# Kernel optimization log

Hardware: AMD Instinct MI355X
Metric: run time of the kernel (lower is better)

The kernel has to match this reference:

```python
import jax, jax.numpy as jnp
import numpy as np

B, L = 4, 2048
D_MODEL, D_STATE, D_CONV, N_BLOCKS = 128, 16, 8, 6
EXPAND = 2
D_INNER = EXPAND * D_MODEL          # 256
DT_RANK = (D_MODEL + 15) // 16      # 8
CONV_K = 7                          # pre_conv kernel


def setup_inputs() -> dict:
    key = jax.random.key(0)
    ks = jax.random.split(key, 10)
    f = lambda k, s: jax.random.normal(k, s, jnp.float32)
    sc = 0.02
    A_init = jnp.broadcast_to(
        jnp.log(jnp.arange(1, D_STATE + 1, dtype=jnp.float32)),
        (N_BLOCKS, D_INNER, D_STATE)) + 0.0
    return {
        "x": f(ks[0], (B, L, 1)),
        "pre_conv_w": f(ks[1], (D_MODEL, 1, CONV_K)) * sc,
        "pre_conv_b": jnp.zeros((D_MODEL,), jnp.float32),
        "ln_w": jnp.ones((N_BLOCKS, D_MODEL), jnp.float32),
        "ln_b": jnp.zeros((N_BLOCKS, D_MODEL), jnp.float32),
        "W_in": f(ks[2], (N_BLOCKS, 2 * D_INNER, D_MODEL)) * sc,
        "conv_w": f(ks[3], (N_BLOCKS, D_INNER, 1, D_CONV)) * sc,  # depthwise OIH
        "conv_b": jnp.zeros((N_BLOCKS, D_INNER), jnp.float32),
        "W_x": f(ks[4], (N_BLOCKS, DT_RANK + 2 * D_STATE, D_INNER)) * sc,
        "W_dt": f(ks[5], (N_BLOCKS, D_INNER, DT_RANK)) * sc,
        "b_dt": jnp.full((N_BLOCKS, D_INNER), -4.6, jnp.float32),  # softplus ~ 0.01
        "A_log": A_init,
        "D_skip": jnp.ones((N_BLOCKS, D_INNER), jnp.float32),
        "W_out": f(ks[6], (N_BLOCKS, D_MODEL, D_INNER)) * sc,
        "out_w": f(ks[7], (1, D_MODEL)) * sc,
        "out_b": jnp.zeros((1,), jnp.float32),
    }


def _layernorm(x, w, b, eps=1e-5):
    m = jnp.mean(x, axis=-1, keepdims=True)
    v = jnp.mean(jnp.square(x - m), axis=-1, keepdims=True)
    return (x - m) * jax.lax.rsqrt(v + eps) * w + b


def _mamba(x, W_in, cw, cb, W_x, W_dt, b_dt, A_log, D_skip, W_out):
    # x: (B, L, D_MODEL)
    xz = jnp.einsum('bld,ed->ble', x, W_in)            # (B,L,2E)
    xi, z = jnp.split(xz, 2, axis=-1)
    # depthwise causal conv over time
    xc = jax.lax.conv_general_dilated(
        xi.transpose(0, 2, 1), cw, window_strides=(1,),
        padding=[(D_CONV - 1, 0)],
        dimension_numbers=('NCH', 'OIH', 'NCH'),
        feature_group_count=D_INNER) + cb[None, :, None]
    xc = jax.nn.silu(xc).transpose(0, 2, 1)            # (B,L,E)
    dbl = jnp.einsum('ble,re->blr', xc, W_x)
    dt = dbl[..., :DT_RANK]
    Bm = dbl[..., DT_RANK:DT_RANK + D_STATE]           # (B,L,N)
    Cm = dbl[..., DT_RANK + D_STATE:]                  # (B,L,N)
    delta = jax.nn.softplus(jnp.einsum('blr,er->ble', dt, W_dt) + b_dt)
    A = -jnp.exp(A_log)                                # (E,N)

    def step(h, inp):
        d, b, c, u = inp                               # (B,E),(B,N),(B,N),(B,E)
        h = h * jnp.exp(d[..., None] * A) + (d * u)[..., None] * b[:, None, :]
        return h, jnp.einsum('ben,bn->be', h, c)

    h0 = jnp.zeros((x.shape[0], D_INNER, D_STATE), x.dtype)
    xs = (delta.transpose(1, 0, 2), Bm.transpose(1, 0, 2),
          Cm.transpose(1, 0, 2), xc.transpose(1, 0, 2))
    _, ys = jax.lax.scan(step, h0, xs)                 # ys: (L,B,E)
    y = ys.transpose(1, 0, 2) + D_skip * xc
    y = y * jax.nn.silu(z)
    return jnp.einsum('ble,de->bld', y, W_out)


def reference(x, pre_conv_w, pre_conv_b, ln_w, ln_b, W_in, conv_w, conv_b,
              W_x, W_dt, b_dt, A_log, D_skip, W_out, out_w, out_b):
    # pre_conv (1 -> d_model), SAME padding, then exact GELU
    h = jax.lax.conv_general_dilated(
        x.transpose(0, 2, 1), pre_conv_w, window_strides=(1,),
        padding=[(CONV_K // 2, CONV_K // 2)],
        dimension_numbers=('NCH', 'OIH', 'NCH')) + pre_conv_b[None, :, None]
    h = jax.nn.gelu(h, approximate=False).transpose(0, 2, 1)  # (B,L,D)

    def block(carry, p):
        lw, lb, Wi, cw, cb, Wx, Wdt, bdt, Alog, Dsk, Wo = p
        y = _mamba(_layernorm(carry, lw, lb), Wi, cw, cb, Wx, Wdt, bdt, Alog, Dsk, Wo)
        return carry + y, None                         # dropout is identity (eval)

    h, _ = jax.lax.scan(block, h, (ln_w, ln_b, W_in, conv_w, conv_b,
                                   W_x, W_dt, b_dt, A_log, D_skip, W_out))
    return (jnp.einsum('bld,od->blo', h, out_w) + out_b)[..., 0]  # (B,L)
```

## Files before the change

### kernel.cpp

```cpp
#include <hip/hip_runtime.h>
#include <hip/hip_bf16.h>
#include <hip/hip_cooperative_groups.h>
#include <math.h>

namespace cg = cooperative_groups;

#define BB 4
#define LL 2048
#define DM 128
#define DI 256
#define DS 16
#define DTR 8
#define NB 6
#define KPRE 7
#define KC 8
#define NC 128
#define CT 16
#define NCHUNK (BB*NC)
#define BL (BB*LL)
#define SU 4

typedef __attribute__((ext_vector_type(8))) short short8v;
typedef __attribute__((ext_vector_type(4))) short short4v;
typedef __attribute__((ext_vector_type(4))) float f32x4;

__device__ __forceinline__ void store_bf16x4(__hip_bfloat16* p, float a, float b, float c, float d) {
    __hip_bfloat16 t[4] = {__float2bfloat16(a), __float2bfloat16(b),
                           __float2bfloat16(c), __float2bfloat16(d)};
    *(short4v*)p = *(const short4v*)t;
}
__device__ __forceinline__ float4 load_bf16x4(const __hip_bfloat16* p) {
    short4v raw = *(const short4v*)p;
    const __hip_bfloat16* t = (const __hip_bfloat16*)&raw;
    return make_float4(__bfloat162float(t[0]), __bfloat162float(t[1]),
                       __bfloat162float(t[2]), __bfloat162float(t[3]));
}
__device__ __forceinline__ void load_bf16x16(const __hip_bfloat16* p, float* o) {
    short8v a = *(const short8v*)p;
    short8v b = *(const short8v*)(p + 8);
    const __hip_bfloat16* ta = (const __hip_bfloat16*)&a;
    const __hip_bfloat16* tb = (const __hip_bfloat16*)&b;
#pragma unroll
    for (int i = 0; i < 8; ++i) { o[i] = __bfloat162float(ta[i]); o[8 + i] = __bfloat162float(tb[i]); }
}
__device__ __forceinline__ void store_bf16x16(__hip_bfloat16* p, const float* v) {
    __hip_bfloat16 t[16];
#pragma unroll
    for (int i = 0; i < 16; ++i) t[i] = __float2bfloat16(v[i]);
    *(short8v*)p = *(const short8v*)t;
    *(short8v*)(p + 8) = *(const short8v*)(t + 8);
}


__device__ __forceinline__ void dev_preconv(int idx,
    const float* __restrict__ x, const float* __restrict__ w, const float* __restrict__ bias,
    float* __restrict__ h, const float* __restrict__ Wi, const float* __restrict__ Wo,
    __hip_bfloat16* __restrict__ wi, __hip_bfloat16* __restrict__ wo) {
    int d = idx & (DM - 1);
    int l = (idx >> 7) & (LL - 1);
    int b = idx >> 18;
    float acc = bias[d];
#pragma unroll
    for (int k = 0; k < KPRE; ++k) {
        int pos = l + k - 3;
        float xv = (pos >= 0 && pos < LL) ? x[b * LL + pos] : 0.f;
        acc = fmaf(xv, w[d * KPRE + k], acc);
    }
    h[idx] = 0.5f * acc * (1.f + erff(acc * 0.70710678118654752f));
    if (idx < NB * 2 * DI * DM) wi[idx] = __float2bfloat16(Wi[idx]);
    if (idx < NB * DM * DI)     wo[idx] = __float2bfloat16(Wo[idx]);
}

__device__ __forceinline__ void dev_phaseA(int chunk, int tid, int epoch,
    const float* __restrict__ h, const float* __restrict__ lw, const float* __restrict__ lb,
    const __hip_bfloat16* __restrict__ Wi,
    const float* __restrict__ cw, const float* __restrict__ cbs,
    const float* __restrict__ Wx, const float* __restrict__ Wdt, const float* __restrict__ bdt,
    const float* __restrict__ A_log,
    __hip_bfloat16* __restrict__ Pst, __hip_bfloat16* __restrict__ hend,
    __hip_bfloat16* __restrict__ hincl, int* __restrict__ flags,
    __hip_bfloat16* As, __hip_bfloat16 (*xi_s)[DI],
    float (*xc_s)[DI], float (*dl_s)[DI], float (*bc_s)[32],
    __hip_bfloat16 (*z_s)[DI], __hip_bfloat16 (*hin_s)[DS]) {
    int c = chunk & (NC - 1);
    int b = chunk >> 7;
    int wave = tid >> 6, lane = tid & 63;
    for (int it = 0; it < 8; ++it) {
        int lr = wave * 8 + it;
        int tl = c * CT + lr - 16;
        int sw = (lr & 7) << 3;
        if (tl >= 0) {
            int t = b * LL + tl;
            float v0 = h[t * DM + lane];
            float v1 = h[t * DM + lane + 64];
            float s = v0 + v1;
#pragma unroll
            for (int off = 32; off; off >>= 1) s += __shfl_xor(s, off);
            float mean = s * (1.f / 128.f);
            float d0 = v0 - mean, d1 = v1 - mean;
            float q = d0 * d0 + d1 * d1;
#pragma unroll
            for (int off = 32; off; off >>= 1) q += __shfl_xor(q, off);
            float rstd = rsqrtf(q * (1.f / 128.f) + 1e-5f);
            As[lr * 128 + (lane ^ sw)]        = __float2bfloat16(d0 * rstd * lw[lane] + lb[lane]);
            As[lr * 128 + ((lane + 64) ^ sw)] = __float2bfloat16(d1 * rstd * lw[lane + 64] + lb[lane + 64]);
        } else {
            As[lr * 128 + (lane ^ sw)]        = __float2bfloat16(0.f);
            As[lr * 128 + ((lane + 64) ^ sw)] = __float2bfloat16(0.f);
        }
    }
    __syncthreads();
    {
        int r = lane & 15, kh = lane >> 4;
        short8v af[2][4];
#pragma unroll
        for (int mf = 0; mf < 2; ++mf)
#pragma unroll
            for (int k = 0; k < 4; ++k) {
                int row = mf * 16 + r;
                int cbk = k * 4 + kh;
                af[mf][k] = *(const short8v*)&As[row * 128 + ((cbk ^ (row & 7)) << 3)];
            }
        int nBase = wave * 128;
        for (int nf = 0; nf < 8; ++nf) {
            short8v bfr[4];
#pragma unroll
            for (int k = 0; k < 4; ++k)
                bfr[k] = *(const short8v*)&Wi[(size_t)(nBase + nf * 16 + r) * DM + k * 32 + kh * 8];
            if (wave < 2) {
                f32x4 acc0 = {}, acc1 = {};
#pragma unroll
                for (int k = 0; k < 4; ++k) {
                    acc0 = __builtin_amdgcn_mfma_f32_16x16x32_bf16(af[0][k], bfr[k], acc0, 0, 0, 0);
                    acc1 = __builtin_amdgcn_mfma_f32_16x16x32_bf16(af[1][k], bfr[k], acc1, 0, 0, 0);
                }
#pragma unroll
                for (int rg = 0; rg < 4; ++rg) {
                    xi_s[kh * 4 + rg][nBase + nf * 16 + r]      = __float2bfloat16(acc0[rg]);
                    xi_s[16 + kh * 4 + rg][nBase + nf * 16 + r] = __float2bfloat16(acc1[rg]);
                }
            } else {
                f32x4 acc1 = {};
#pragma unroll
                for (int k = 0; k < 4; ++k)
                    acc1 = __builtin_amdgcn_mfma_f32_16x16x32_bf16(af[1][k], bfr[k], acc1, 0, 0, 0);
#pragma unroll
                for (int rg = 0; rg < 4; ++rg)
                    z_s[kh * 4 + rg][(nBase - 256) + nf * 16 + r] = __float2bfloat16(acc1[rg]);
            }
        }
    }
    __syncthreads();
    for (int i = 0; i < 4; ++i) {
        int lt = wave * 4 + i;
        float xv[4];
        for (int j = 0; j < 4; ++j) {
            int e = lane + 64 * j;
            float4 c0 = *(const float4*)&cw[e * KC];
            float4 c1 = *(const float4*)&cw[e * KC + 4];
            float wts[8] = {c0.x, c0.y, c0.z, c0.w, c1.x, c1.y, c1.z, c1.w};
            float acc = cbs[e];
#pragma unroll
            for (int k = 0; k < KC; ++k)
                acc = fmaf(__bfloat162float(xi_s[lt + 9 + k][e]), wts[k], acc);
            xv[j] = acc / (1.f + __expf(-acc));
            xc_s[lt][e] = xv[j];
        }
        float dt8[8];
        float bcv = 0.f;
#pragma unroll
        for (int o = 0; o < 40; ++o) {
            const float* w = &Wx[o * DI];
            float s = xv[0] * w[lane];
            s = fmaf(xv[1], w[lane + 64], s);
            s = fmaf(xv[2], w[lane + 128], s);
            s = fmaf(xv[3], w[lane + 192], s);
#pragma unroll
            for (int off = 32; off; off >>= 1) s += __shfl_xor(s, off);
            if (o < 8) dt8[o] = s;
            else if (lane == o - 8) bcv = s;
        }
        if (lane < 32) bc_s[lt][lane] = bcv;
        for (int j = 0; j < 4; ++j) {
            int e = lane + 64 * j;
            float s = bdt[e];
#pragma unroll
            for (int r = 0; r < 8; ++r) s = fmaf(dt8[r], Wdt[e * 8 + r], s);
            dl_s[lt][e] = fmaxf(s, 0.f) + log1pf(__expf(-fabsf(s)));
        }
    }
    __syncthreads();
    int e = tid;
    {
        float d16[CT], u16[CT];
#pragma unroll
        for (int l = 0; l < CT; ++l) { d16[l] = dl_s[l][e]; u16[l] = xc_s[l][e]; }
        for (int ng = 0; ng < 4; ++ng) {
            float4 al = *(const float4*)&A_log[e * DS + 4 * ng];
            float Aen[4] = {-__expf(al.x), -__expf(al.y), -__expf(al.z), -__expf(al.w)};
            float hh[4] = {}, Pl[4] = {1.f, 1.f, 1.f, 1.f};
#pragma unroll
            for (int l = 0; l < CT; ++l) {
                float du = d16[l] * u16[l];
                float4 bm = *(const float4*)&bc_s[l][4 * ng];
                float a0 = __expf(d16[l] * Aen[0]);
                float a1 = __expf(d16[l] * Aen[1]);
                float a2 = __expf(d16[l] * Aen[2]);
                float a3 = __expf(d16[l] * Aen[3]);
                hh[0] = fmaf(hh[0], a0, du * bm.x);
                hh[1] = fmaf(hh[1], a1, du * bm.y);
                hh[2] = fmaf(hh[2], a2, du * bm.z);
                hh[3] = fmaf(hh[3], a3, du * bm.w);
                Pl[0] *= a0; Pl[1] *= a1; Pl[2] *= a2; Pl[3] *= a3;
            }
            size_t oidx = (((size_t)(b * NC + c)) * DI + e) * DS + 4 * ng;
            store_bf16x4(&Pst[oidx], Pl[0], Pl[1], Pl[2], Pl[3]);
            store_bf16x4(&hend[oidx], hh[0], hh[1], hh[2], hh[3]);
        }
    }
    __threadfence();
    __syncthreads();
    if (tid == 0)
        __hip_atomic_store(&flags[b * NC + c], 2 * epoch,
                           __ATOMIC_RELEASE, __HIP_MEMORY_SCOPE_AGENT);
    float hacc[16], Pacc[16];
#pragma unroll
    for (int n = 0; n < 16; ++n) { hacc[n] = 0.f; Pacc[n] = 1.f; }
    int j = c - 1;
    while (j >= 0) {
        int j2 = (j >= 1) ? j - 1 : j;
        int f1, f0;
        do {
            f1 = __hip_atomic_load(&flags[b * NC + j],  __ATOMIC_ACQUIRE, __HIP_MEMORY_SCOPE_AGENT);
            f0 = __hip_atomic_load(&flags[b * NC + j2], __ATOMIC_ACQUIRE, __HIP_MEMORY_SCOPE_AGENT);
            if (f1 < 2 * epoch || f0 < 2 * epoch) __builtin_amdgcn_s_sleep(2);
        } while (f1 < 2 * epoch || f0 < 2 * epoch);
        size_t bj = (((size_t)(b * NC + j)) * DI + e) * DS;
        if (f1 > 2 * epoch) {
            float hi[16]; load_bf16x16(&hincl[bj], hi);
#pragma unroll
            for (int n = 0; n < 16; ++n) hacc[n] = fmaf(Pacc[n], hi[n], hacc[n]);
            break;
        }
        float pj[16], he[16];
        load_bf16x16(&Pst[bj], pj);
        load_bf16x16(&hend[bj], he);
#pragma unroll
        for (int n = 0; n < 16; ++n) { hacc[n] = fmaf(Pacc[n], he[n], hacc[n]); Pacc[n] *= pj[n]; }
        if (j == 0) break;
        size_t bj0 = (((size_t)(b * NC + j - 1)) * DI + e) * DS;
        if (f0 > 2 * epoch) {
            float hi[16]; load_bf16x16(&hincl[bj0], hi);
#pragma unroll
            for (int n = 0; n < 16; ++n) hacc[n] = fmaf(Pacc[n], hi[n], hacc[n]);
            break;
        }
        float pj0[16], he0[16];
        load_bf16x16(&Pst[bj0], pj0);
        load_bf16x16(&hend[bj0], he0);
#pragma unroll
        for (int n = 0; n < 16; ++n) { hacc[n] = fmaf(Pacc[n], he0[n], hacc[n]); Pacc[n] *= pj0[n]; }
        j -= 2;
    }
    {
        size_t bcx = (((size_t)(b * NC + c)) * DI + e) * DS;
        float pc[16], hc[16];
        load_bf16x16(&Pst[bcx], pc);
        load_bf16x16(&hend[bcx], hc);
#pragma unroll
        for (int n = 0; n < 16; ++n) {
            hin_s[e][n] = __float2bfloat16(hacc[n]);
            hc[n] = fmaf(pc[n], hacc[n], hc[n]);
        }
        store_bf16x16(&hincl[bcx], hc);
    }
    __threadfence();
    __syncthreads();
    if (tid == 0)
        __hip_atomic_store(&flags[b * NC + c], 2 * epoch + 1,
                           __ATOMIC_RELEASE, __HIP_MEMORY_SCOPE_AGENT);
}

__device__ __forceinline__ void dev_fusedB(int chunk, int tid,
    const float* __restrict__ A_log, const float* __restrict__ Dsk,
    const __hip_bfloat16* __restrict__ Wo, float* __restrict__ hout,
    const float (*xc_s)[DI], const float (*dl_s)[DI], const float (*bc_s)[32],
    const __hip_bfloat16 (*z_s)[DI], const __hip_bfloat16 (*hin_s)[DS],
    __hip_bfloat16 (*y_s)[DI + 8]) {
    int c = chunk & (NC - 1);
    int b = chunk >> 7;
    int base = b * LL + c * CT;
    int e = tid;
    float d16[CT], u16[CT], yacc[CT];
    float dsk = Dsk[e];
#pragma unroll
    for (int l = 0; l < CT; ++l) {
        d16[l] = dl_s[l][e];
        u16[l] = xc_s[l][e];
        yacc[l] = dsk * u16[l];
    }
    for (int ng = 0; ng < 4; ++ng) {
        float4 al = *(const float4*)&A_log[e * DS + 4 * ng];
        float Aen[4] = {-__expf(al.x), -__expf(al.y), -__expf(al.z), -__expf(al.w)};
        float hh[4] = {__bfloat162float(hin_s[e][4 * ng]),
                       __bfloat162float(hin_s[e][4 * ng + 1]),
                       __bfloat162float(hin_s[e][4 * ng + 2]),
                       __bfloat162float(hin_s[e][4 * ng + 3])};
#pragma unroll
        for (int l = 0; l < CT; ++l) {
            float du = d16[l] * u16[l];
            float4 bm = *(const float4*)&bc_s[l][4 * ng];
            float4 cm = *(const float4*)&bc_s[l][16 + 4 * ng];
            float a0 = __expf(d16[l] * Aen[0]);
            float a1 = __expf(d16[l] * Aen[1]);
            float a2 = __expf(d16[l] * Aen[2]);
            float a3 = __expf(d16[l] * Aen[3]);
            hh[0] = fmaf(hh[0], a0, du * bm.x);
            hh[1] = fmaf(hh[1], a1, du * bm.y);
            hh[2] = fmaf(hh[2], a2, du * bm.z);
            hh[3] = fmaf(hh[3], a3, du * bm.w);
            float p = hh[0] * cm.x;
            p = fmaf(hh[1], cm.y, p);
            p = fmaf(hh[2], cm.z, p);
            p = fmaf(hh[3], cm.w, p);
            yacc[l] += p;
        }
    }
#pragma unroll
    for (int l = 0; l < CT; ++l) {
        float z = __bfloat162float(z_s[l][e]);
        y_s[l][e] = __float2bfloat16(yacc[l] * (z / (1.f + __expf(-z))));
    }
    __syncthreads();
    int wave = tid >> 6, lane = tid & 63;
    int r  = lane & 15;
    int kh = lane >> 4;
    f32x4 acc[2] = {};
    for (int k0 = 0; k0 < DI; k0 += 32) {
        short8v af = *(const short8v*)&y_s[r][k0 + kh * 8];
        short8v bf[2];
#pragma unroll
        for (int jj = 0; jj < 2; ++jj)
            bf[jj] = *(const short8v*)&Wo[(size_t)(wave * 32 + jj * 16 + r) * DI + k0 + kh * 8];
#pragma unroll
        for (int jj = 0; jj < 2; ++jj)
            acc[jj] = __builtin_amdgcn_mfma_f32_16x16x32_bf16(af, bf[jj], acc[jj], 0, 0, 0);
    }
    __syncthreads();
#pragma unroll
    for (int jj = 0; jj < 2; ++jj)
#pragma unroll
        for (int rg = 0; rg < 4; ++rg) {
            size_t off = (size_t)(base + kh * 4 + rg) * DM + wave * 32 + jj * 16 + r;
            hout[off] += acc[jj][rg];
        }
}

__device__ __forceinline__ void dev_out(int t, int lane,
    const float* __restrict__ h, const float* __restrict__ ow, const float* __restrict__ ob,
    float* __restrict__ out) {
    float s = h[t * DM + lane] * ow[lane] + h[t * DM + lane + 64] * ow[lane + 64];
#pragma unroll
    for (int off = 32; off; off >>= 1) s += __shfl_xor(s, off);
    if (lane == 0) out[t] = s + ob[0];
}


__device__ __forceinline__ void dev_ln_gemm1(int v, int wave, int lane,
    const float* __restrict__ h, const float* __restrict__ lw, const float* __restrict__ lb,
    const __hip_bfloat16* __restrict__ W, float* __restrict__ xz,
    __hip_bfloat16* As) {
    int tileM = v >> 2, tileN = v & 3;
    int mBase = tileM * 64, nBase = tileN * 128;
    for (int it = 0; it < 16; ++it) {
        int row = wave * 16 + it;
        int t = mBase + row;
        float v0 = h[t * DM + lane];
        float v1 = h[t * DM + lane + 64];
        float s = v0 + v1;
#pragma unroll
        for (int off = 32; off; off >>= 1) s += __shfl_xor(s, off);
        float mean = s * (1.f / 128.f);
        float d0 = v0 - mean, d1 = v1 - mean;
        float q = d0 * d0 + d1 * d1;
#pragma unroll
        for (int off = 32; off; off >>= 1) q += __shfl_xor(q, off);
        float rstd = rsqrtf(q * (1.f / 128.f) + 1e-5f);
        int sw = (row & 7) << 3;
        As[row * 128 + (lane ^ sw)]        = __float2bfloat16(d0 * rstd * lw[lane] + lb[lane]);
        As[row * 128 + ((lane + 64) ^ sw)] = __float2bfloat16(d1 * rstd * lw[lane + 64] + lb[lane + 64]);
    }
    __syncthreads();
    int r  = lane & 15;
    int kh = lane >> 4;
    f32x4 acc[4][2] = {};
    for (int k0 = 0; k0 < DM; k0 += 32) {
        short8v af[4], bf[2];
#pragma unroll
        for (int i = 0; i < 4; ++i) {
            int row = i * 16 + r;
            int cbk = (k0 >> 3) + kh;
            af[i] = *(const short8v*)&As[row * 128 + ((cbk ^ (row & 7)) << 3)];
        }
#pragma unroll
        for (int j = 0; j < 2; ++j)
            bf[j] = *(const short8v*)&W[(size_t)(nBase + wave * 32 + j * 16 + r) * DM + k0 + kh * 8];
#pragma unroll
        for (int i = 0; i < 4; ++i)
#pragma unroll
            for (int j = 0; j < 2; ++j)
                acc[i][j] = __builtin_amdgcn_mfma_f32_16x16x32_bf16(af[i], bf[j], acc[i][j], 0, 0, 0);
    }
#pragma unroll
    for (int i = 0; i < 4; ++i)
#pragma unroll
        for (int j = 0; j < 2; ++j)
#pragma unroll
            for (int rg = 0; rg < 4; ++rg) {
                size_t off = (size_t)(mBase + i * 16 + kh * 4 + rg) * (2 * DI)
                           + nBase + wave * 32 + j * 16 + r;
                xz[off] = acc[i][j][rg];
            }
    __syncthreads();
}

__device__ __forceinline__ void dev_conv_wx(int t, int lane,
    const float* __restrict__ xz, const float* __restrict__ cw, const float* __restrict__ cbs,
    const float* __restrict__ Wx, const float* __restrict__ Wdt, const float* __restrict__ bdt,
    float* __restrict__ xc, float* __restrict__ BC, float* __restrict__ delta) {
    int tl = t & (LL - 1);
    int b = t >> 11;
    float xv[4];
#pragma unroll
    for (int j = 0; j < 4; ++j) {
        int e = lane + 64 * j;
        float4 cw0 = *(const float4*)&cw[e * KC];
        float4 cw1 = *(const float4*)&cw[e * KC + 4];
        float wts[8] = {cw0.x, cw0.y, cw0.z, cw0.w, cw1.x, cw1.y, cw1.z, cw1.w};
        float acc = cbs[e];
#pragma unroll
        for (int k = 0; k < KC; ++k) {
            int pos = tl + k - (KC - 1);
            float v = (pos >= 0) ? xz[((size_t)(b * LL + pos) << 9) + e] : 0.f;
            acc = fmaf(v, wts[k], acc);
        }
        xv[j] = acc / (1.f + __expf(-acc));
        xc[((size_t)t << 8) + e] = xv[j];
    }
    float dt[8];
    float bcv = 0.f;
#pragma unroll
    for (int o = 0; o < 40; ++o) {
        const float* w = &Wx[o * DI];
        float s = xv[0] * w[lane];
        s = fmaf(xv[1], w[lane + 64], s);
        s = fmaf(xv[2], w[lane + 128], s);
        s = fmaf(xv[3], w[lane + 192], s);
#pragma unroll
        for (int off = 32; off; off >>= 1) s += __shfl_xor(s, off);
        if (o < 8) dt[o] = s;
        else if (lane == o - 8) bcv = s;
    }
    if (lane < 32) BC[((size_t)t << 5) + lane] = bcv;
#pragma unroll
    for (int j = 0; j < 4; ++j) {
        int e = lane + 64 * j;
        float s = bdt[e];
#pragma unroll
        for (int r = 0; r < 8; ++r) s = fmaf(dt[r], Wdt[e * 8 + r], s);
        delta[((size_t)t << 8) + e] = fmaxf(s, 0.f) + log1pf(__expf(-fabsf(s)));
    }
}

__device__ __forceinline__ void dev_scan1(int blk, int tid,
    const float* __restrict__ delta, const float* __restrict__ xc, const float* __restrict__ BC,
    const float* __restrict__ A_log,
    __hip_bfloat16* __restrict__ P, __hip_bfloat16* __restrict__ hend) {
    int eg = blk & 3;
    int c = (blk >> 2) & (NC - 1);
    int b = blk >> 9;
    int e = eg * 64 + (tid >> 2);
    int ng = tid & 3;
    float4 al = *(const float4*)&A_log[e * DS + 4 * ng];
    float Aen[4] = {-__expf(al.x), -__expf(al.y), -__expf(al.z), -__expf(al.w)};
    float h[4] = {}, Pl[4] = {1.f, 1.f, 1.f, 1.f};
    int base = b * LL + c * CT;
    const float* dp = delta + (size_t)base * DI + e;
    const float* up = xc + (size_t)base * DI + e;
    const float* bp = BC + (size_t)base * 32 + 4 * ng;
    for (int l0 = 0; l0 < CT; l0 += SU) {
        float d[SU], u[SU];
        float4 bm[SU];
#pragma unroll
        for (int j = 0; j < SU; ++j) {
            d[j]  = dp[(l0 + j) * DI];
            u[j]  = up[(l0 + j) * DI];
            bm[j] = *(const float4*)&bp[(l0 + j) * 32];
        }
#pragma unroll
        for (int j = 0; j < SU; ++j) {
            float du = d[j] * u[j];
            float a0 = __expf(d[j] * Aen[0]);
            float a1 = __expf(d[j] * Aen[1]);
            float a2 = __expf(d[j] * Aen[2]);
            float a3 = __expf(d[j] * Aen[3]);
            h[0] = fmaf(h[0], a0, du * bm[j].x);
            h[1] = fmaf(h[1], a1, du * bm[j].y);
            h[2] = fmaf(h[2], a2, du * bm[j].z);
            h[3] = fmaf(h[3], a3, du * bm[j].w);
            Pl[0] *= a0; Pl[1] *= a1; Pl[2] *= a2; Pl[3] *= a3;
        }
    }
    size_t oidx = (((size_t)(b * NC + c)) * DI + e) * DS + 4 * ng;
    store_bf16x4(&P[oidx], Pl[0], Pl[1], Pl[2], Pl[3]);
    store_bf16x4(&hend[oidx], h[0], h[1], h[2], h[3]);
}

__device__ __forceinline__ void dev_carry(int gtid,
    const __hip_bfloat16* __restrict__ P, const __hip_bfloat16* __restrict__ hend,
    __hip_bfloat16* __restrict__ hin) {
    int n = gtid & 15;
    int e = (gtid >> 4) & 255;
    int b = gtid >> 12;
    const size_t cs = (size_t)DI * DS;
    size_t idx0 = (((size_t)(b * NC)) * DI + e) * DS + n;
    float carry = 0.f;
    for (int c0 = 0; c0 < NC; c0 += 8) {
        float p[8], he[8];
#pragma unroll
        for (int j = 0; j < 8; ++j) {
            size_t idx = idx0 + (size_t)(c0 + j) * cs;
            p[j]  = __bfloat162float(P[idx]);
            he[j] = __bfloat162float(hend[idx]);
        }
#pragma unroll
        for (int j = 0; j < 8; ++j) {
            hin[idx0 + (size_t)(c0 + j) * cs] = __float2bfloat16(carry);
            carry = fmaf(p[j], carry, he[j]);
        }
    }
}

__device__ __forceinline__ void dev_scan3(int blk, int tid,
    const float* __restrict__ delta, const float* __restrict__ xc, const float* __restrict__ BC,
    const float* __restrict__ A_log, const __hip_bfloat16* __restrict__ hin,
    const float* __restrict__ xz,
    const float* __restrict__ Dsk, __hip_bfloat16* __restrict__ y) {
    int eg = blk & 3;
    int c = (blk >> 2) & (NC - 1);
    int b = blk >> 9;
    int e = eg * 64 + (tid >> 2);
    int ng = tid & 3;
    float4 al = *(const float4*)&A_log[e * DS + 4 * ng];
    float Aen[4] = {-__expf(al.x), -__expf(al.y), -__expf(al.z), -__expf(al.w)};
    float dsk = Dsk[e];
    float4 h4 = load_bf16x4(&hin[(((size_t)(b * NC + c)) * DI + e) * DS + 4 * ng]);
    float h[4] = {h4.x, h4.y, h4.z, h4.w};
    int base = b * LL + c * CT;
    const float* dp = delta + (size_t)base * DI + e;
    const float* up = xc + (size_t)base * DI + e;
    const float* bp = BC + (size_t)base * 32 + 4 * ng;
    const float* zp = xz + ((size_t)base << 9) + DI + e;
    __hip_bfloat16* yp = y + (size_t)base * DI + e;
    for (int l0 = 0; l0 < CT; l0 += SU) {
        float d[SU], u[SU], zv[SU];
        float4 bm[SU], cm[SU];
#pragma unroll
        for (int j = 0; j < SU; ++j) {
            d[j]  = dp[(l0 + j) * DI];
            u[j]  = up[(l0 + j) * DI];
            bm[j] = *(const float4*)&bp[(l0 + j) * 32];
            cm[j] = *(const float4*)&bp[(l0 + j) * 32 + 16];
            zv[j] = zp[(size_t)(l0 + j) << 9];
        }
#pragma unroll
        for (int j = 0; j < SU; ++j) {
            float du = d[j] * u[j];
            float a0 = __expf(d[j] * Aen[0]);
            float a1 = __expf(d[j] * Aen[1]);
            float a2 = __expf(d[j] * Aen[2]);
            float a3 = __expf(d[j] * Aen[3]);
            h[0] = fmaf(h[0], a0, du * bm[j].x);
            h[1] = fmaf(h[1], a1, du * bm[j].y);
            h[2] = fmaf(h[2], a2, du * bm[j].z);
            h[3] = fmaf(h[3], a3, du * bm[j].w);
            float yc = h[0] * cm[j].x;
            yc = fmaf(h[1], cm[j].y, yc);
            yc = fmaf(h[2], cm[j].z, yc);
            yc = fmaf(h[3], cm[j].w, yc);
            yc += __shfl_xor(yc, 1);
            yc += __shfl_xor(yc, 2);
            if (ng == 0) {
                float z = zv[j];
                float val = (yc + dsk * u[j]) * (z / (1.f + __expf(-z)));
                yp[(l0 + j) * DI] = __float2bfloat16(val);
            }
        }
    }
}

__device__ __forceinline__ void dev_gemm2(int v, int wave, int lane,
    const __hip_bfloat16* __restrict__ A, const __hip_bfloat16* __restrict__ W,
    float* __restrict__ C) {
    int mBase = v * 16;
    int r  = lane & 15;
    int kh = lane >> 4;
    f32x4 acc[2] = {};
    for (int k0 = 0; k0 < DI; k0 += 32) {
        short8v af = *(const short8v*)&A[(size_t)(mBase + r) * DI + k0 + kh * 8];
        short8v bf[2];
#pragma unroll
        for (int j = 0; j < 2; ++j)
            bf[j] = *(const short8v*)&W[(size_t)(wave * 32 + j * 16 + r) * DI + k0 + kh * 8];
#pragma unroll
        for (int j = 0; j < 2; ++j)
            acc[j] = __builtin_amdgcn_mfma_f32_16x16x32_bf16(af, bf[j], acc[j], 0, 0, 0);
    }
#pragma unroll
    for (int j = 0; j < 2; ++j)
#pragma unroll
        for (int rg = 0; rg < 4; ++rg) {
            size_t off = (size_t)(mBase + kh * 4 + rg) * DM + wave * 32 + j * 16 + r;
            C[off] += acc[j][rg];
        }
}


struct MegaArgs {
    const float *x, *pcw, *pcb, *ln_w, *ln_b, *conv_w, *conv_b;
    const float *W_x, *W_dt, *b_dt, *A_log, *D_skip, *W_in, *W_out, *out_w, *out_b;
    float *h, *out;
    __hip_bfloat16 *P, *hend, *hincl, *wi_bf, *wo_bf;
    int *flags;
};

__global__ __launch_bounds__(256, 2) void k_mega(MegaArgs a) {
    __shared__ union {
        struct {
            __hip_bfloat16 As[32 * 128];
            __hip_bfloat16 xi[32][DI];
        } pa;
        __hip_bfloat16 y_s[CT][DI + 8];
    } u;
    __shared__ float xc_s[CT][DI];
    __shared__ float dl_s[CT][DI];
    __shared__ float bc_s[CT][32];
    __shared__ __hip_bfloat16 z_s[CT][DI];
    __shared__ __hip_bfloat16 hin_s[DI][DS];
    cg::grid_group g = cg::this_grid();
    int bid = blockIdx.x, tid = threadIdx.x;
    int nb = gridDim.x;
    int wave = tid >> 6, lane = tid & 63;

    for (int v = bid * 256 + tid; v < NCHUNK; v += nb * 256) a.flags[v] = 0;
    for (int v = bid; v < (BB * LL * DM) / 256; v += nb)
        dev_preconv(v * 256 + tid, a.x, a.pcw, a.pcb, a.h, a.W_in, a.W_out, a.wi_bf, a.wo_bf);
    g.sync();

    for (int blk = 0; blk < NB; ++blk) {
        dev_phaseA(bid, tid, blk + 1, a.h, a.ln_w + blk * DM, a.ln_b + blk * DM,
                   a.wi_bf + (size_t)blk * 2 * DI * DM,
                   a.conv_w + (size_t)blk * DI * KC, a.conv_b + blk * DI,
                   a.W_x + (size_t)blk * 40 * DI, a.W_dt + (size_t)blk * DI * DTR,
                   a.b_dt + blk * DI, a.A_log + (size_t)blk * DI * DS,
                   a.P, a.hend, a.hincl, a.flags,
                   u.pa.As, u.pa.xi, xc_s, dl_s, bc_s, z_s, hin_s);
        dev_fusedB(bid, tid, a.A_log + (size_t)blk * DI * DS,
                   a.D_skip + blk * DI, a.wo_bf + (size_t)blk * DM * DI, a.h,
                   xc_s, dl_s, bc_s, z_s, hin_s, u.y_s);
        g.sync();
    }

    for (int v = bid; v < BL / 4; v += nb)
        dev_out(v * 4 + wave, lane, a.h, a.out_w, a.out_b, a.out);
}


__global__ void w_preconv(const float* x, const float* w, const float* bias, float* h,
                          const float* Wi, const float* Wo,
                          __hip_bfloat16* wi, __hip_bfloat16* wo) {
    dev_preconv(blockIdx.x * 256 + threadIdx.x, x, w, bias, h, Wi, Wo, wi, wo);
}
__global__ __launch_bounds__(256) void w_ln_gemm1(const float* h, const float* lw, const float* lb,
                                                  const __hip_bfloat16* W, float* xz) {
    __shared__ __hip_bfloat16 As[64 * 128];
    dev_ln_gemm1(blockIdx.x, threadIdx.x >> 6, threadIdx.x & 63, h, lw, lb, W, xz, As);
}
__global__ __launch_bounds__(256) void w_conv_wx(const float* xz, const float* cw, const float* cbs,
                                                 const float* Wx, const float* Wdt, const float* bdt,
                                                 float* xc, float* BC, float* delta) {
    dev_conv_wx(blockIdx.x * 4 + (threadIdx.x >> 6), threadIdx.x & 63,
                xz, cw, cbs, Wx, Wdt, bdt, xc, BC, delta);
}
__global__ __launch_bounds__(256) void w_scan1(const float* delta, const float* xc, const float* BC,
                                               const float* A_log,
                                               __hip_bfloat16* P, __hip_bfloat16* hend) {
    dev_scan1(blockIdx.x, threadIdx.x, delta, xc, BC, A_log, P, hend);
}
__global__ void w_carry(const __hip_bfloat16* P, const __hip_bfloat16* hend, __hip_bfloat16* hin) {
    dev_carry(blockIdx.x * 256 + threadIdx.x, P, hend, hin);
}
__global__ __launch_bounds__(256) void w_scan3(const float* delta, const float* xc, const float* BC,
                                               const float* A_log, const __hip_bfloat16* hin,
                                               const float* xz,
                                               const float* Dsk, __hip_bfloat16* y) {
    dev_scan3(blockIdx.x, threadIdx.x, delta, xc, BC, A_log, hin, xz, Dsk, y);
}
__global__ __launch_bounds__(256) void w_gemm2(const __hip_bfloat16* A, const __hip_bfloat16* W,
                                               float* C) {
    dev_gemm2(blockIdx.x, threadIdx.x >> 6, threadIdx.x & 63, A, W, C);
}
__global__ void w_out(const float* h, const float* ow, const float* ob, float* out) {
    dev_out(blockIdx.x * 4 + (threadIdx.x >> 6), threadIdx.x & 63, h, ow, ob, out);
}

extern "C" void kernel_launch(void* const* d_in, const int* in_sizes, int n_in,
                              void* d_out, int out_size, void* d_ws, size_t ws_size,
                              hipStream_t stream) {
    (void)in_sizes; (void)n_in; (void)out_size; (void)ws_size;
    const float* x      = (const float*)d_in[0];
    const float* pcw    = (const float*)d_in[1];
    const float* pcb    = (const float*)d_in[2];
    const float* ln_w   = (const float*)d_in[3];
    const float* ln_b   = (const float*)d_in[4];
    const float* W_in   = (const float*)d_in[5];
    const float* conv_w = (const float*)d_in[6];
    const float* conv_b = (const float*)d_in[7];
    const float* W_x    = (const float*)d_in[8];
    const float* W_dt   = (const float*)d_in[9];
    const float* b_dt   = (const float*)d_in[10];
    const float* A_log  = (const float*)d_in[11];
    const float* D_skip = (const float*)d_in[12];
    const float* W_out  = (const float*)d_in[13];
    const float* out_w  = (const float*)d_in[14];
    const float* out_b  = (const float*)d_in[15];

    const size_t SCAN_N = (size_t)BB * NC * DI * DS;
    float* ws    = (float*)d_ws;
    float* h     = ws;
    float* xz    = h     + (size_t)BL * DM;
    float* xc    = xz    + (size_t)BL * 2 * DI;
    float* BC    = xc    + (size_t)BL * DI;
    float* delta = BC    + (size_t)BL * 2 * DS;
    __hip_bfloat16* P     = (__hip_bfloat16*)(delta + (size_t)BL * DI);
    __hip_bfloat16* hend  = P + SCAN_N;
    __hip_bfloat16* hin   = hend + SCAN_N;
    __hip_bfloat16* hincl = hin + SCAN_N;
    __hip_bfloat16* y_bf  = hincl + SCAN_N;
    __hip_bfloat16* wi_bf = y_bf + (size_t)BL * DI;
    __hip_bfloat16* wo_bf = wi_bf + (size_t)NB * 2 * DI * DM;
    int* flags = (int*)(wo_bf + (size_t)NB * DM * DI);

    int dev = 0;
    (void)hipGetDevice(&dev);
    int coopAttr = 0;
    (void)hipDeviceGetAttribute(&coopAttr, hipDeviceAttributeCooperativeLaunch, dev);
    int numCU = 0;
    (void)hipDeviceGetAttribute(&numCU, hipDeviceAttributeMultiprocessorCount, dev);
    int maxBpCU = 0;
    (void)hipOccupancyMaxActiveBlocksPerMultiprocessor(&maxBpCU, k_mega, 256, 0);
    int grid = maxBpCU * numCU;
    if (grid > NCHUNK) grid = NCHUNK;

    bool launched = false;
    if (coopAttr && grid == NCHUNK) {
        MegaArgs ma = {x, pcw, pcb, ln_w, ln_b, conv_w, conv_b,
                       W_x, W_dt, b_dt, A_log, D_skip, W_in, W_out, out_w, out_b,
                       h, (float*)d_out,
                       P, hend, hincl, wi_bf, wo_bf, flags};
        void* kp[] = {&ma};
        hipError_t e = hipLaunchCooperativeKernel((void*)k_mega, dim3(grid), dim3(256), kp, 0, stream);
        launched = (e == hipSuccess);
        if (!launched) (void)hipGetLastError();
    }

    if (!launched) {
        w_preconv<<<(BB * LL * DM) / 256, 256, 0, stream>>>(x, pcw, pcb, h, W_in, W_out, wi_bf, wo_bf);
        for (int blk = 0; blk < NB; ++blk) {
            w_ln_gemm1<<<512, 256, 0, stream>>>(
                h, ln_w + blk * DM, ln_b + blk * DM, wi_bf + (size_t)blk * 2 * DI * DM, xz);
            w_conv_wx<<<BL / 4, 256, 0, stream>>>(
                xz, conv_w + (size_t)blk * DI * KC, conv_b + blk * DI,
                W_x + (size_t)blk * 40 * DI, W_dt + (size_t)blk * DI * DTR,
                b_dt + blk * DI, xc, BC, delta);
            w_scan1<<<BB * NC * 4, 256, 0, stream>>>(
                delta, xc, BC, A_log + (size_t)blk * DI * DS, P, hend);
            w_carry<<<(BB * DI * DS) / 256, 256, 0, stream>>>(P, hend, hin);
            w_scan3<<<BB * NC * 4, 256, 0, stream>>>(
                delta, xc, BC, A_log + (size_t)blk * DI * DS, hin, xz, D_skip + blk * DI, y_bf);
            w_gemm2<<<BL / 16, 256, 0, stream>>>(y_bf, wo_bf + (size_t)blk * DM * DI, h);
        }
        w_out<<<BL / 4, 256, 0, stream>>>(h, out_w, out_b, (float*)d_out);
    }
}
```

Before: 562.5 us.

## Double megakernel block size to 512 threads and use MFMA for x_proj

New measurement: 554.1 us. Within noise of the previous version (-1.5%).

```diff
diff --git a/kernel.cpp b/kernel.cpp
--- a/kernel.cpp
+++ b/kernel.cpp
@@ -35,27 +35,26 @@
     return make_float4(__bfloat162float(t[0]), __bfloat162float(t[1]),
                        __bfloat162float(t[2]), __bfloat162float(t[3]));
 }
-__device__ __forceinline__ void load_bf16x16(const __hip_bfloat16* p, float* o) {
+__device__ __forceinline__ void load_bf16x8(const __hip_bfloat16* p, float* o) {
     short8v a = *(const short8v*)p;
-    short8v b = *(const short8v*)(p + 8);
     const __hip_bfloat16* ta = (const __hip_bfloat16*)&a;
-    const __hip_bfloat16* tb = (const __hip_bfloat16*)&b;
-#pragma unroll
-    for (int i = 0; i < 8; ++i) { o[i] = __bfloat162float(ta[i]); o[8 + i] = __bfloat162float(tb[i]); }
-}
-__device__ __forceinline__ void store_bf16x16(__hip_bfloat16* p, const float* v) {
-    __hip_bfloat16 t[16];
-#pragma unroll
-    for (int i = 0; i < 16; ++i) t[i] = __float2bfloat16(v[i]);
+#pragma unroll
+    for (int i = 0; i < 8; ++i) o[i] = __bfloat162float(ta[i]);
+}
+__device__ __forceinline__ void store_bf16x8(__hip_bfloat16* p, const float* v) {
+    __hip_bfloat16 t[8];
+#pragma unroll
+    for (int i = 0; i < 8; ++i) t[i] = __float2bfloat16(v[i]);
     *(short8v*)p = *(const short8v*)t;
-    *(short8v*)(p + 8) = *(const short8v*)(t + 8);
 }
 
 
 __device__ __forceinline__ void dev_preconv(int idx,
     const float* __restrict__ x, const float* __restrict__ w, const float* __restrict__ bias,
     float* __restrict__ h, const float* __restrict__ Wi, const float* __restrict__ Wo,
-    __hip_bfloat16* __restrict__ wi, __hip_bfloat16* __restrict__ wo) {
+    const float* __restrict__ Wxf,
+    __hip_bfloat16* __restrict__ wi, __hip_bfloat16* __restrict__ wo,
+    __hip_bfloat16* __restrict__ wx) {
     int d = idx & (DM - 1);
     int l = (idx >> 7) & (LL - 1);
     int b = idx >> 18;
@@ -69,24 +68,25 @@
     h[idx] = 0.5f * acc * (1.f + erff(acc * 0.70710678118654752f));
     if (idx < NB * 2 * DI * DM) wi[idx] = __float2bfloat16(Wi[idx]);
     if (idx < NB * DM * DI)     wo[idx] = __float2bfloat16(Wo[idx]);
+    if (idx < NB * 40 * DI)     wx[idx] = __float2bfloat16(Wxf[idx]);
 }
 
 __device__ __forceinline__ void dev_phaseA(int chunk, int tid, int epoch,
     const float* __restrict__ h, const float* __restrict__ lw, const float* __restrict__ lb,
-    const __hip_bfloat16* __restrict__ Wi,
+    const __hip_bfloat16* __restrict__ Wi, const __hip_bfloat16* __restrict__ Wx,
     const float* __restrict__ cw, const float* __restrict__ cbs,
-    const float* __restrict__ Wx, const float* __restrict__ Wdt, const float* __restrict__ bdt,
+    const float* __restrict__ Wdt, const float* __restrict__ bdt,
     const float* __restrict__ A_log,
     __hip_bfloat16* __restrict__ Pst, __hip_bfloat16* __restrict__ hend,
     __hip_bfloat16* __restrict__ hincl, int* __restrict__ flags,
     __hip_bfloat16* As, __hip_bfloat16 (*xi_s)[DI],
-    float (*xc_s)[DI], float (*dl_s)[DI], float (*bc_s)[32],
-    __hip_bfloat16 (*z_s)[DI], __hip_bfloat16 (*hin_s)[DS]) {
+    __hip_bfloat16 (*xcb_s)[DI], float (*dl_s)[DI], float (*bc_s)[32],
+    __hip_bfloat16 (*z_s)[DI], __hip_bfloat16 (*hin_s)[DS], float (*dbl_s)[48]) {
     int c = chunk & (NC - 1);
     int b = chunk >> 7;
     int wave = tid >> 6, lane = tid & 63;
-    for (int it = 0; it < 8; ++it) {
-        int lr = wave * 8 + it;
+    for (int it = 0; it < 4; ++it) {
+        int lr = wave * 4 + it;
         int tl = c * CT + lr - 16;
         int sw = (lr & 7) << 3;
         if (tl >= 0) {
@@ -121,13 +121,13 @@
                 int cbk = k * 4 + kh;
                 af[mf][k] = *(const short8v*)&As[row * 128 + ((cbk ^ (row & 7)) << 3)];
             }
-        int nBase = wave * 128;
-        for (int nf = 0; nf < 8; ++nf) {
-            short8v bfr[4];
-#pragma unroll
-            for (int k = 0; k < 4; ++k)
-                bfr[k] = *(const short8v*)&Wi[(size_t)(nBase + nf * 16 + r) * DM + k * 32 + kh * 8];
-            if (wave < 2) {
+        if (wave < 4) {
+            int nBase = wave * 64;
+            for (int nf = 0; nf < 4; ++nf) {
+                short8v bfr[4];
+#pragma unroll
+                for (int k = 0; k < 4; ++k)
+                    bfr[k] = *(const short8v*)&Wi[(size_t)(nBase + nf * 16 + r) * DM + k * 32 + kh * 8];
                 f32x4 acc0 = {}, acc1 = {};
 #pragma unroll
                 for (int k = 0; k < 4; ++k) {
@@ -139,21 +139,28 @@
                     xi_s[kh * 4 + rg][nBase + nf * 16 + r]      = __float2bfloat16(acc0[rg]);
                     xi_s[16 + kh * 4 + rg][nBase + nf * 16 + r] = __float2bfloat16(acc1[rg]);
                 }
-            } else {
+            }
+        } else {
+            int zBase = (wave - 4) * 64;
+            for (int nf = 0; nf < 4; ++nf) {
+                short8v bfr[4];
+#pragma unroll
+                for (int k = 0; k < 4; ++k)
+                    bfr[k] = *(const short8v*)&Wi[(size_t)(256 + zBase + nf * 16 + r) * DM + k * 32 + kh * 8];
                 f32x4 acc1 = {};
 #pragma unroll
                 for (int k = 0; k < 4; ++k)
                     acc1 = __builtin_amdgcn_mfma_f32_16x16x32_bf16(af[1][k], bfr[k], acc1, 0, 0, 0);
 #pragma unroll
                 for (int rg = 0; rg < 4; ++rg)
-                    z_s[kh * 4 + rg][(nBase - 256) + nf * 16 + r] = __float2bfloat16(acc1[rg]);
+                    z_s[kh * 4 + rg][zBase + nf * 16 + r] = __float2bfloat16(acc1[rg]);
             }
         }
     }
     __syncthreads();
-    for (int i = 0; i < 4; ++i) {
-        int lt = wave * 4 + i;
-        float xv[4];
+    for (int i = 0; i < 2; ++i) {
+        int lt = wave * 2 + i;
+#pragma unroll
         for (int j = 0; j < 4; ++j) {
             int e = lane + 64 * j;
             float4 c0 = *(const float4*)&cw[e * KC];
@@ -163,39 +170,48 @@
 #pragma unroll
             for (int k = 0; k < KC; ++k)
                 acc = fmaf(__bfloat162float(xi_s[lt + 9 + k][e]), wts[k], acc);
-            xv[j] = acc / (1.f + __expf(-acc));
-            xc_s[lt][e] = xv[j];
-        }
-        float dt8[8];
-        float bcv = 0.f;
-#pragma unroll
-        for (int o = 0; o < 40; ++o) {
-            const float* w = &Wx[o * DI];
-            float s = xv[0] * w[lane];
-            s = fmaf(xv[1], w[lane + 64], s);
-            s = fmaf(xv[2], w[lane + 128], s);
-            s = fmaf(xv[3], w[lane + 192], s);
-#pragma unroll
-            for (int off = 32; off; off >>= 1) s += __shfl_xor(s, off);
-            if (o < 8) dt8[o] = s;
-            else if (lane == o - 8) bcv = s;
-        }
-        if (lane < 32) bc_s[lt][lane] = bcv;
-        for (int j = 0; j < 4; ++j) {
-            int e = lane + 64 * j;
+            float sv = acc / (1.f + __expf(-acc));
+            xcb_s[lt][e] = __float2bfloat16(sv);
+        }
+    }
+    __syncthreads();
+    if (wave < 3) {
+        int r = lane & 15, kh = lane >> 4;
+        f32x4 acc = {};
+        for (int k0 = 0; k0 < DI; k0 += 32) {
+            short8v a = *(const short8v*)&xcb_s[r][k0 + kh * 8];
+            int o = wave * 16 + r;
+            short8v w8;
+            if (o < 40) w8 = *(const short8v*)&Wx[(size_t)o * DI + k0 + kh * 8];
+            else { short z[8] = {}; w8 = *(const short8v*)z; }
+            acc = __builtin_amdgcn_mfma_f32_16x16x32_bf16(a, w8, acc, 0, 0, 0);
+        }
+#pragma unroll
+        for (int rg = 0; rg < 4; ++rg)
+            dbl_s[kh * 4 + rg][wave * 16 + r] = acc[rg];
+    }
+    __syncthreads();
+    {
+        int l = tid >> 5, i = tid & 31;
+        bc_s[l][i] = dbl_s[l][8 + i];
+    }
+    {
+        int e = tid & 255, th = tid >> 8;
+        for (int l = th * 8; l < th * 8 + 8; ++l) {
             float s = bdt[e];
 #pragma unroll
-            for (int r = 0; r < 8; ++r) s = fmaf(dt8[r], Wdt[e * 8 + r], s);
-            dl_s[lt][e] = fmaxf(s, 0.f) + log1pf(__expf(-fabsf(s)));
-        }
-    }
-    __syncthreads();
-    int e = tid;
+            for (int r = 0; r < 8; ++r) s = fmaf(dbl_s[l][r], Wdt[e * 8 + r], s);
+            dl_s[l][e] = fmaxf(s, 0.f) + log1pf(__expf(-fabsf(s)));
+        }
+    }
+    __syncthreads();
+    int e = tid >> 1, half = tid & 1;
     {
         float d16[CT], u16[CT];
 #pragma unroll
-        for (int l = 0; l < CT; ++l) { d16[l] = dl_s[l][e]; u16[l] = xc_s[l][e]; }
-        for (int ng = 0; ng < 4; ++ng) {
+        for (int l = 0; l < CT; ++l) { d16[l] = dl_s[l][e]; u16[l] = __bfloat162float(xcb_s[l][e]); }
+        for (int ngi = 0; ngi < 2; ++ngi) {
+            int ng = half * 2 + ngi;
             float4 al = *(const float4*)&A_log[e * DS + 4 * ng];
             float Aen[4] = {-__expf(al.x), -__expf(al.y), -__expf(al.z), -__expf(al.w)};
             float hh[4] = {}, Pl[4] = {1.f, 1.f, 1.f, 1.f};
@@ -223,56 +239,41 @@
     if (tid == 0)
         __hip_atomic_store(&flags[b * NC + c], 2 * epoch,
                            __ATOMIC_RELEASE, __HIP_MEMORY_SCOPE_AGENT);
-    float hacc[16], Pacc[16];
-#pragma unroll
-    for (int n = 0; n < 16; ++n) { hacc[n] = 0.f; Pacc[n] = 1.f; }
+    float hacc[8], Pacc[8];
+#pragma unroll
+    for (int n = 0; n < 8; ++n) { hacc[n] = 0.f; Pacc[n] = 1.f; }
     int j = c - 1;
     while (j >= 0) {
-        int j2 = (j >= 1) ? j - 1 : j;
-        int f1, f0;
+        int f1;
         do {
-            f1 = __hip_atomic_load(&flags[b * NC + j],  __ATOMIC_ACQUIRE, __HIP_MEMORY_SCOPE_AGENT);
-            f0 = __hip_atomic_load(&flags[b * NC + j2], __ATOMIC_ACQUIRE, __HIP_MEMORY_SCOPE_AGENT);
-            if (f1 < 2 * epoch || f0 < 2 * epoch) __builtin_amdgcn_s_sleep(2);
-        } while (f1 < 2 * epoch || f0 < 2 * epoch);
-        size_t bj = (((size_t)(b * NC + j)) * DI + e) * DS;
+            f1 = __hip_atomic_load(&flags[b * NC + j], __ATOMIC_ACQUIRE, __HIP_MEMORY_SCOPE_AGENT);
+            if (f1 < 2 * epoch) __builtin_amdgcn_s_sleep(2);
+        } while (f1 < 2 * epoch);
+        size_t bj = (((size_t)(b * NC + j)) * DI + e) * DS + half * 8;
         if (f1 > 2 * epoch) {
-            float hi[16]; load_bf16x16(&hincl[bj], hi);
-#pragma unroll
-            for (int n = 0; n < 16; ++n) hacc[n] = fmaf(Pacc[n], hi[n], hacc[n]);
+            float hi[8]; load_bf16x8(&hincl[bj], hi);
+#pragma unroll
+            for (int n = 0; n < 8; ++n) hacc[n] = fmaf(Pacc[n], hi[n], hacc[n]);
             break;
         }
-        float pj[16], he[16];
-        load_bf16x16(&Pst[bj], pj);
-        load_bf16x16(&hend[bj], he);
-#pragma unroll
-        for (int n = 0; n < 16; ++n) { hacc[n] = fmaf(Pacc[n], he[n], hacc[n]); Pacc[n] *= pj[n]; }
-        if (j == 0) break;
-        size_t bj0 = (((size_t)(b * NC + j - 1)) * DI + e) * DS;
-        if (f0 > 2 * epoch) {
-            float hi[16]; load_bf16x16(&hincl[bj0], hi);
-#pragma unroll
-            for (int n = 0; n < 16; ++n) hacc[n] = fmaf(Pacc[n], hi[n], hacc[n]);
-            break;
-        }
-        float pj0[16], he0[16];
-        load_bf16x16(&Pst[bj0], pj0);
-        load_bf16x16(&hend[bj0], he0);
-#pragma unroll
-        for (int n = 0; n < 16; ++n) { hacc[n] = fmaf(Pacc[n], he0[n], hacc[n]); Pacc[n] *= pj0[n]; }
-        j -= 2;
+        float pj[8], he[8];
+        load_bf16x8(&Pst[bj], pj);
+        load_bf16x8(&hend[bj], he);
+#pragma unroll
+        for (int n = 0; n < 8; ++n) { hacc[n] = fmaf(Pacc[n], he[n], hacc[n]); Pacc[n] *= pj[n]; }
+        --j;
     }
     {
-        size_t bcx = (((size_t)(b * NC + c)) * DI + e) * DS;
-        float pc[16], hc[16];
-        load_bf16x16(&Pst[bcx], pc);
-        load_bf16x16(&hend[bcx], hc);
-#pragma unroll
-        for (int n = 0; n < 16; ++n) {
-            hin_s[e][n] = __float2bfloat16(hacc[n]);
+        size_t bcx = (((size_t)(b * NC + c)) * DI + e) * DS + half * 8;
+        float pc[8], hc[8];
+        load_bf16x8(&Pst[bcx], pc);
+        load_bf16x8(&hend[bcx], hc);
+#pragma unroll
+        for (int n = 0; n < 8; ++n) {
+            hin_s[e][half * 8 + n] = __float2bfloat16(hacc[n]);
             hc[n] = fmaf(pc[n], hacc[n], hc[n]);
         }
-        store_bf16x16(&hincl[bcx], hc);
+        store_bf16x8(&hincl[bcx], hc);
     }
     __threadfence();
     __syncthreads();
@@ -284,22 +285,23 @@
 __device__ __forceinline__ void dev_fusedB(int chunk, int tid,
     const float* __restrict__ A_log, const float* __restrict__ Dsk,
     const __hip_bfloat16* __restrict__ Wo, float* __restrict__ hout,
-    const float (*xc_s)[DI], const float (*dl_s)[DI], const float (*bc_s)[32],
+    const __hip_bfloat16 (*xcb_s)[DI], const float (*dl_s)[DI], const float (*bc_s)[32],
     const __hip_bfloat16 (*z_s)[DI], const __hip_bfloat16 (*hin_s)[DS],
     __hip_bfloat16 (*y_s)[DI + 8]) {
     int c = chunk & (NC - 1);
     int b = chunk >> 7;
     int base = b * LL + c * CT;
-    int e = tid;
+    int e = tid >> 1, half = tid & 1;
     float d16[CT], u16[CT], yacc[CT];
     float dsk = Dsk[e];
 #pragma unroll
     for (int l = 0; l < CT; ++l) {
         d16[l] = dl_s[l][e];
-        u16[l] = xc_s[l][e];
-        yacc[l] = dsk * u16[l];
-    }
-    for (int ng = 0; ng < 4; ++ng) {
+        u16[l] = __bfloat162float(xcb_s[l][e]);
+        yacc[l] = half ? 0.f : dsk * u16[l];
+    }
+    for (int ngi = 0; ngi < 2; ++ngi) {
+        int ng = half * 2 + ngi;
         float4 al = *(const float4*)&A_log[e * DS + 4 * ng];
         float Aen[4] = {-__expf(al.x), -__expf(al.y), -__expf(al.z), -__expf(al.w)};
         float hh[4] = {__bfloat162float(hin_s[e][4 * ng]),
@@ -328,32 +330,28 @@
     }
 #pragma unroll
     for (int l = 0; l < CT; ++l) {
-        float z = __bfloat162float(z_s[l][e]);
-        y_s[l][e] = __float2bfloat16(yacc[l] * (z / (1.f + __expf(-z))));
+        float full = yacc[l] + __shfl_xor(yacc[l], 1);
+        if (half == 0) {
+            float z = __bfloat162float(z_s[l][e]);
+            y_s[l][e] = __float2bfloat16(full * (z / (1.f + __expf(-z))));
+        }
     }
     __syncthreads();
     int wave = tid >> 6, lane = tid & 63;
     int r  = lane & 15;
     int kh = lane >> 4;
-    f32x4 acc[2] = {};
+    f32x4 acc = {};
     for (int k0 = 0; k0 < DI; k0 += 32) {
         short8v af = *(const short8v*)&y_s[r][k0 + kh * 8];
-        short8v bf[2];
-#pragma unroll
-        for (int jj = 0; jj < 2; ++jj)
-            bf[jj] = *(const short8v*)&Wo[(size_t)(wave * 32 + jj * 16 + r) * DI + k0 + kh * 8];
-#pragma unroll
-        for (int jj = 0; jj < 2; ++jj)
-            acc[jj] = __builtin_amdgcn_mfma_f32_16x16x32_bf16(af, bf[jj], acc[jj], 0, 0, 0);
-    }
-    __syncthreads();
-#pragma unroll
-    for (int jj = 0; jj < 2; ++jj)
-#pragma unroll
-        for (int rg = 0; rg < 4; ++rg) {
-            size_t off = (size_t)(base + kh * 4 + rg) * DM + wave * 32 + jj * 16 + r;
-            hout[off] += acc[jj][rg];
-        }
+        short8v bf = *(const short8v*)&Wo[(size_t)(wave * 16 + r) * DI + k0 + kh * 8];
+        acc = __builtin_amdgcn_mfma_f32_16x16x32_bf16(af, bf, acc, 0, 0, 0);
+    }
+    __syncthreads();
+#pragma unroll
+    for (int rg = 0; rg < 4; ++rg) {
+        size_t off = (size_t)(base + kh * 4 + rg) * DM + wave * 16 + r;
+        hout[off] += acc[rg];
+    }
 }
 
 __device__ __forceinline__ void dev_out(int t, int lane,
@@ -366,10 +364,83 @@
 }
 
 
-__device__ __forceinline__ void dev_ln_gemm1(int v, int wave, int lane,
-    const float* __restrict__ h, const float* __restrict__ lw, const float* __restrict__ lb,
-    const __hip_bfloat16* __restrict__ W, float* __restrict__ xz,
-    __hip_bfloat16* As) {
+struct MegaArgs {
+    const float *x, *pcw, *pcb, *ln_w, *ln_b, *conv_w, *conv_b;
+    const float *W_x, *W_dt, *b_dt, *A_log, *D_skip, *W_in, *W_out, *out_w, *out_b;
+    float *h, *out;
+    __hip_bfloat16 *P, *hend, *hincl, *wi_bf, *wo_bf, *wx_bf;
+    int *flags;
+};
+
+__global__ __launch_bounds__(512, 2) void k_mega(MegaArgs a) {
+    __shared__ union {
+        struct {
+            __hip_bfloat16 As[32 * 128];
+            __hip_bfloat16 xi[32][DI];
+        } pa;
+        __hip_bfloat16 y_s[CT][DI + 8];
+    } u;
+    __shared__ __hip_bfloat16 xcb_s[CT][DI];
+    __shared__ float dl_s[CT][DI];
+    __shared__ float bc_s[CT][32];
+    __shared__ __hip_bfloat16 z_s[CT][DI];
+    __shared__ __hip_bfloat16 hin_s[DI][DS];
+    __shared__ float dbl_s[CT][48];
+    cg::grid_group g = cg::this_grid();
+    int bid = blockIdx.x, tid = threadIdx.x;
+    int nb = gridDim.x;
+    int wave = tid >> 6, lane = tid & 63;
+
+    for (int v = bid * 512 + tid; v < NCHUNK; v += nb * 512) a.flags[v] = 0;
+    for (int v = bid; v < (BB * LL * DM) / 512; v += nb)
+        dev_preconv(v * 512 + tid, a.x, a.pcw, a.pcb, a.h, a.W_in, a.W_out, a.W_x,
+                    a.wi_bf, a.wo_bf, a.wx_bf);
+    g.sync();
+
+    for (int blk = 0; blk < NB; ++blk) {
+        dev_phaseA(bid, tid, blk + 1, a.h, a.ln_w + blk * DM, a.ln_b + blk * DM,
+                   a.wi_bf + (size_t)blk * 2 * DI * DM, a.wx_bf + (size_t)blk * 40 * DI,
+                   a.conv_w + (size_t)blk * DI * KC, a.conv_b + blk * DI,
+                   a.W_dt + (size_t)blk * DI * DTR, a.b_dt + blk * DI,
+                   a.A_log + (size_t)blk * DI * DS,
+                   a.P, a.hend, a.hincl, a.flags,
+                   u.pa.As, u.pa.xi, xcb_s, dl_s, bc_s, z_s, hin_s, dbl_s);
+        dev_fusedB(bid, tid, a.A_log + (size_t)blk * DI * DS,
+                   a.D_skip + blk * DI, a.wo_bf + (size_t)blk * DM * DI, a.h,
+                   xcb_s, dl_s, bc_s, z_s, hin_s, u.y_s);
+        g.sync();
+    }
+
+    for (int v = bid; v < BL / 8; v += nb)
+        dev_out(v * 8 + wave, lane, a.h, a.out_w, a.out_b, a.out);
+}
+
+
+__global__ void w_preconv(const float* x, const float* w, const float* bias, float* h,
+                          const float* Wi, const float* Wo, const float* Wxf,
+                          __hip_bfloat16* wi, __hip_bfloat16* wo, __hip_bfloat16* wx) {
+    int idx = blockIdx.x * 256 + threadIdx.x;
+    int d = idx & (DM - 1);
+    int l = (idx >> 7) & (LL - 1);
+    int b = idx >> 18;
+    float acc = bias[d];
+#pragma unroll
+    for (int k = 0; k < KPRE; ++k) {
+        int pos = l + k - 3;
+        float xv = (pos >= 0 && pos < LL) ? x[b * LL + pos] : 0.f;
+        acc = fmaf(xv, w[d * KPRE + k], acc);
+    }
+    h[idx] = 0.5f * acc * (1.f + erff(acc * 0.70710678118654752f));
+    if (idx < NB * 2 * DI * DM) wi[idx] = __float2bfloat16(Wi[idx]);
+    if (idx < NB * DM * DI)     wo[idx] = __float2bfloat16(Wo[idx]);
+    if (idx < NB * 40 * DI)     wx[idx] = __float2bfloat16(Wxf[idx]);
+}
+
+__global__ __launch_bounds__(256) void w_ln_gemm1(const float* __restrict__ h,
+    const float* __restrict__ lw, const float* __restrict__ lb,
+    const __hip_bfloat16* __restrict__ W, float* __restrict__ xz) {
+    __shared__ __hip_bfloat16 As[64 * 128];
+    int v = blockIdx.x, wave = threadIdx.x >> 6, lane = threadIdx.x & 63;
     int tileM = v >> 2, tileN = v & 3;
     int mBase = tileM * 64, nBase = tileN * 128;
     for (int it = 0; it < 16; ++it) {
@@ -421,13 +492,14 @@
                            + nBase + wave * 32 + j * 16 + r;
                 xz[off] = acc[i][j][rg];
             }
-    __syncthreads();
-}
-
-__device__ __forceinline__ void dev_conv_wx(int t, int lane,
-    const float* __restrict__ xz, const float* __restrict__ cw, const float* __restrict__ cbs,
+}
+
+__global__ __launch_bounds__(256) void w_conv_wx(const float* __restrict__ xz,
+    const float* __restrict__ cw, const float* __restrict__ cbs,
     const float* __restrict__ Wx, const float* __restrict__ Wdt, const float* __restrict__ bdt,
     float* __restrict__ xc, float* __restrict__ BC, float* __restrict__ delta) {
+    int lane = threadIdx.x & 63;
+    int t = blockIdx.x * 4 + (threadIdx.x >> 6);
     int tl = t & (LL - 1);
     int b = t >> 11;
     float xv[4];
@@ -472,10 +544,11 @@
     }
 }
 
-__device__ __forceinline__ void dev_scan1(int blk, int tid,
-    const float* __restrict__ delta, const float* __restrict__ xc, const float* __restrict__ BC,
+__global__ __launch_bounds__(256) void w_scan1(const float* __restrict__ delta,
+    const float* __restrict__ xc, const float* __restrict__ BC,
     const float* __restrict__ A_log,
     __hip_bfloat16* __restrict__ P, __hip_bfloat16* __restrict__ hend) {
+    int blk = blockIdx.x, tid = threadIdx.x;
     int eg = blk & 3;
     int c = (blk >> 2) & (NC - 1);
     int b = blk >> 9;
@@ -489,17 +562,17 @@
     const float* up = xc + (size_t)base * DI + e;
     const float* bp = BC + (size_t)base * 32 + 4 * ng;
     for (int l0 = 0; l0 < CT; l0 += SU) {
-        float d[SU], u[SU];
+        float d[SU], uu[SU];
         float4 bm[SU];
 #pragma unroll
         for (int j = 0; j < SU; ++j) {
             d[j]  = dp[(l0 + j) * DI];
-            u[j]  = up[(l0 + j) * DI];
+            uu[j] = up[(l0 + j) * DI];
             bm[j] = *(const float4*)&bp[(l0 + j) * 32];
         }
 #pragma unroll
         for (int j = 0; j < SU; ++j) {
-            float du = d[j] * u[j];
+            float du = d[j] * uu[j];
             float a0 = __expf(d[j] * Aen[0]);
             float a1 = __expf(d[j] * Aen[1]);
             float a2 = __expf(d[j] * Aen[2]);
@@ -516,9 +589,10 @@
     store_bf16x4(&hend[oidx], h[0], h[1], h[2], h[3]);
 }
 
-__device__ __forceinline__ void dev_carry(int gtid,
-    const __hip_bfloat16* __restrict__ P, const __hip_bfloat16* __restrict__ hend,
-    __hip_bfloat16* __restrict__ hin) {
+__global__ void w_carry(const __hip_bfloat16* __restrict__ P,
+                        const __hip_bfloat16* __restrict__ hend,
+                        __hip_bfloat16* __restrict__ hin) {
+    int gtid = blockIdx.x * 256 + threadIdx.x;
     int n = gtid & 15;
     int e = (gtid >> 4) & 255;
     int b = gtid >> 12;
@@ -541,11 +615,12 @@
     }
 }
 
-__device__ __forceinline__ void dev_scan3(int blk, int tid,
-    const float* __restrict__ delta, const float* __restrict__ xc, const float* __restrict__ BC,
+__global__ __launch_bounds__(256) void w_scan3(const float* __restrict__ delta,
+    const float* __restrict__ xc, const float* __restrict__ BC,
     const float* __restrict__ A_log, const __hip_bfloat16* __restrict__ hin,
     const float* __restrict__ xz,
     const float* __restrict__ Dsk, __hip_bfloat16* __restrict__ y) {
+    int blk = blockIdx.x, tid = threadIdx.x;
     int eg = blk & 3;
     int c = (blk >> 2) & (NC - 1);
     int b = blk >> 9;
@@ -563,19 +638,19 @@
     const float* zp = xz + ((size_t)base << 9) + DI + e;
     __hip_bfloat16* yp = y + (size_t)base * DI + e;
     for (int l0 = 0; l0 < CT; l0 += SU) {
-        float d[SU], u[SU], zv[SU];
+        float d[SU], uu[SU], zv[SU];
         float4 bm[SU], cm[SU];
 #pragma unroll
         for (int j = 0; j < SU; ++j) {
             d[j]  = dp[(l0 + j) * DI];
-            u[j]  = up[(l0 + j) * DI];
+            uu[j] = up[(l0 + j) * DI];
             bm[j] = *(const float4*)&bp[(l0 + j) * 32];
             cm[j] = *(const float4*)&bp[(l0 + j) * 32 + 16];
             zv[j] = zp[(size_t)(l0 + j) << 9];
         }
 #pragma unroll
         for (int j = 0; j < SU; ++j) {
-            float du = d[j] * u[j];
+            float du = d[j] * uu[j];
             float a0 = __expf(d[j] * Aen[0]);
             float a1 = __expf(d[j] * Aen[1]);
             float a2 = __expf(d[j] * Aen[2]);
@@ -592,16 +667,17 @@
             yc += __shfl_xor(yc, 2);
             if (ng == 0) {
                 float z = zv[j];
-                float val = (yc + dsk * u[j]) * (z / (1.f + __expf(-z)));
+                float val = (yc + dsk * uu[j]) * (z / (1.f + __expf(-z)));
                 yp[(l0 + j) * DI] = __float2bfloat16(val);
             }
         }
     }
 }
 
-__device__ __forceinline__ void dev_gemm2(int v, int wave, int lane,
-    const __hip_bfloat16* __restrict__ A, const __hip_bfloat16* __restrict__ W,
-    float* __restrict__ C) {
+__global__ __launch_bounds__(256) void w_gemm2(const __hip_bfloat16* __restrict__ A,
+                                               const __hip_bfloat16* __restrict__ W,
+                                               float* __restrict__ C) {
+    int v = blockIdx.x, wave = threadIdx.x >> 6, lane = threadIdx.x & 63;
     int mBase = v * 16;
     int r  = lane & 15;
     int kh = lane >> 4;
@@ -625,91 +701,6 @@
         }
 }
 
-
-struct MegaArgs {
-    const float *x, *pcw, *pcb, *ln_w, *ln_b, *conv_w, *conv_b;
-    const float *W_x, *W_dt, *b_dt, *A_log, *D_skip, *W_in, *W_out, *out_w, *out_b;
-    float *h, *out;
-    __hip_bfloat16 *P, *hend, *hincl, *wi_bf, *wo_bf;
-    int *flags;
-};
-
-__global__ __launch_bounds__(256, 2) void k_mega(MegaArgs a) {
-    __shared__ union {
-        struct {
-            __hip_bfloat16 As[32 * 128];
-            __hip_bfloat16 xi[32][DI];
-        } pa;
-        __hip_bfloat16 y_s[CT][DI + 8];
-    } u;
-    __shared__ float xc_s[CT][DI];
-    __shared__ float dl_s[CT][DI];
-    __shared__ float bc_s[CT][32];
-    __shared__ __hip_bfloat16 z_s[CT][DI];
-    __shared__ __hip_bfloat16 hin_s[DI][DS];
-    cg::grid_group g = cg::this_grid();
-    int bid = blockIdx.x, tid = threadIdx.x;
-    int nb = gridDim.x;
-    int wave = tid >> 6, lane = tid & 63;
-
-    for (int v = bid * 256 + tid; v < NCHUNK; v += nb * 256) a.flags[v] = 0;
-    for (int v = bid; v < (BB * LL * DM) / 256; v += nb)
-        dev_preconv(v * 256 + tid, a.x, a.pcw, a.pcb, a.h, a.W_in, a.W_out, a.wi_bf, a.wo_bf);
-    g.sync();
-
-    for (int blk = 0; blk < NB; ++blk) {
-        dev_phaseA(bid, tid, blk + 1, a.h, a.ln_w + blk * DM, a.ln_b + blk * DM,
-                   a.wi_bf + (size_t)blk * 2 * DI * DM,
-                   a.conv_w + (size_t)blk * DI * KC, a.conv_b + blk * DI,
-                   a.W_x + (size_t)blk * 40 * DI, a.W_dt + (size_t)blk * DI * DTR,
-                   a.b_dt + blk * DI, a.A_log + (size_t)blk * DI * DS,
-                   a.P, a.hend, a.hincl, a.flags,
-                   u.pa.As, u.pa.xi, xc_s, dl_s, bc_s, z_s, hin_s);
-        dev_fusedB(bid, tid, a.A_log + (size_t)blk * DI * DS,
-                   a.D_skip + blk * DI, a.wo_bf + (size_t)blk * DM * DI, a.h,
-                   xc_s, dl_s, bc_s, z_s, hin_s, u.y_s);
-        g.sync();
-    }
-
-    for (int v = bid; v < BL / 4; v += nb)
-        dev_out(v * 4 + wave, lane, a.h, a.out_w, a.out_b, a.out);
-}
-
-
-__global__ void w_preconv(const float* x, const float* w, const float* bias, float* h,
-                          const float* Wi, const float* Wo,
-                          __hip_bfloat16* wi, __hip_bfloat16* wo) {
-    dev_preconv(blockIdx.x * 256 + threadIdx.x, x, w, bias, h, Wi, Wo, wi, wo);
-}
-__global__ __launch_bounds__(256) void w_ln_gemm1(const float* h, const float* lw, const float* lb,
-                                                  const __hip_bfloat16* W, float* xz) {
-    __shared__ __hip_bfloat16 As[64 * 128];
-    dev_ln_gemm1(blockIdx.x, threadIdx.x >> 6, threadIdx.x & 63, h, lw, lb, W, xz, As);
-}
-__global__ __launch_bounds__(256) void w_conv_wx(const float* xz, const float* cw, const float* cbs,
-                                                 const float* Wx, const float* Wdt, const float* bdt,
-                                                 float* xc, float* BC, float* delta) {
-    dev_conv_wx(blockIdx.x * 4 + (threadIdx.x >> 6), threadIdx.x & 63,
-                xz, cw, cbs, Wx, Wdt, bdt, xc, BC, delta);
-}
-__global__ __launch_bounds__(256) void w_scan1(const float* delta, const float* xc, const float* BC,
-                                               const float* A_log,
-                                               __hip_bfloat16* P, __hip_bfloat16* hend) {
-    dev_scan1(blockIdx.x, threadIdx.x, delta, xc, BC, A_log, P, hend);
-}
-__global__ void w_carry(const __hip_bfloat16* P, const __hip_bfloat16* hend, __hip_bfloat16* hin) {
-    dev_carry(blockIdx.x * 256 + threadIdx.x, P, hend, hin);
-}
-__global__ __launch_bounds__(256) void w_scan3(const float* delta, const float* xc, const float* BC,
-                                               const float* A_log, const __hip_bfloat16* hin,
-                                               const float* xz,
-                                               const float* Dsk, __hip_bfloat16* y) {
-    dev_scan3(blockIdx.x, threadIdx.x, delta, xc, BC, A_log, hin, xz, Dsk, y);
-}
-__global__ __launch_bounds__(256) void w_gemm2(const __hip_bfloat16* A, const __hip_bfloat16* W,
-                                               float* C) {
-    dev_gemm2(blockIdx.x, threadIdx.x >> 6, threadIdx.x & 63, A, W, C);
-}
 __global__ void w_out(const float* h, const float* ow, const float* ob, float* out) {
     dev_out(blockIdx.x * 4 + (threadIdx.x >> 6), threadIdx.x & 63, h, ow, ob, out);
 }
@@ -749,7 +740,8 @@
     __hip_bfloat16* y_bf  = hincl + SCAN_N;
     __hip_bfloat16* wi_bf = y_bf + (size_t)BL * DI;
     __hip_bfloat16* wo_bf = wi_bf + (size_t)NB * 2 * DI * DM;
-    int* flags = (int*)(wo_bf + (size_t)NB * DM * DI);
+    __hip_bfloat16* wx_bf = wo_bf + (size_t)NB * DM * DI;
+    int* flags = (int*)(wx_bf + (size_t)NB * 40 * DI);
 
     int dev = 0;
     (void)hipGetDevice(&dev);
@@ -758,7 +750,7 @@
     int numCU = 0;
     (void)hipDeviceGetAttribute(&numCU, hipDeviceAttributeMultiprocessorCount, dev);
     int maxBpCU = 0;
-    (void)hipOccupancyMaxActiveBlocksPerMultiprocessor(&maxBpCU, k_mega, 256, 0);
+    (void)hipOccupancyMaxActiveBlocksPerMultiprocessor(&maxBpCU, k_mega, 512, 0);
     int grid = maxBpCU * numCU;
     if (grid > NCHUNK) grid = NCHUNK;
 
@@ -767,15 +759,16 @@
         MegaArgs ma = {x, pcw, pcb, ln_w, ln_b, conv_w, conv_b,
                        W_x, W_dt, b_dt, A_log, D_skip, W_in, W_out, out_w, out_b,
                        h, (float*)d_out,
-                       P, hend, hincl, wi_bf, wo_bf, flags};
+                       P, hend, hincl, wi_bf, wo_bf, wx_bf, flags};
         void* kp[] = {&ma};
-        hipError_t e = hipLaunchCooperativeKernel((void*)k_mega, dim3(grid), dim3(256), kp, 0, stream);
+        hipError_t e = hipLaunchCooperativeKernel((void*)k_mega, dim3(grid), dim3(512), kp, 0, stream);
         launched = (e == hipSuccess);
         if (!launched) (void)hipGetLastError();
     }
 
     if (!launched) {
-        w_preconv<<<(BB * LL * DM) / 256, 256, 0, stream>>>(x, pcw, pcb, h, W_in, W_out, wi_bf, wo_bf);
+        w_preconv<<<(BB * LL * DM) / 256, 256, 0, stream>>>(
+            x, pcw, pcb, h, W_in, W_out, W_x, wi_bf, wo_bf, wx_bf);
         for (int blk = 0; blk < NB; ++blk) {
             w_ln_gemm1<<<512, 256, 0, stream>>>(
                 h, ln_w + blk * DM, ln_b + blk * DM, wi_bf + (size_t)blk * 2 * DI * DM, xz);
```
